# Performance work log

Hardware: AMD Instinct MI355X
Metric: run time of the kernel (lower is better)

The kernel has to match this reference:

```python
import jax, jax.numpy as jnp
import numpy as np

PRUNE = 5      # prune_range from __init__
NEG = -1e30    # finite stand-in for -inf (avoids NaN grads)


def setup_inputs() -> dict:
    B, T, U, V = 8, 200, 200, 512
    key = jax.random.key(0)
    k1, k2, k3, k4 = jax.random.split(key, 4)
    logits = jax.random.normal(k1, (B, T, U, V), dtype=jnp.float32)
    log_probs = jax.nn.log_softmax(logits, axis=-1)  # module expects log_softmax output
    targets = jax.random.randint(k2, (B, U), 1, V, dtype=jnp.int32)  # 0 is blank
    # t_len <= T-1 required since DP indexes log_probs[b, t_len, ...]
    logit_lengths = jax.random.randint(k3, (B,), 120, T, dtype=jnp.int32)
    # diagonal band pruning => need |u_len - t_len| <= PRUNE for finite loss
    target_lengths = logit_lengths - jax.random.randint(k4, (B,), 0, PRUNE + 1, dtype=jnp.int32)
    return {
        "log_probs": log_probs,
        "targets": targets,
        "logit_lengths": logit_lengths,
        "target_lengths": target_lengths,
    }


def _alpha_grid(lp, tgt):
    """Banded RNNT forward DP for one sample.

    lp: (T, U, V) log-probs, tgt: (U,) int labels.
    Returns alpha grid of shape (T, U); alpha[t, u] matches the torch loop
    (cells outside the band u in [t-P, t+P] are NEG).
    """
    T, U, V = lp.shape
    u = jnp.arange(U)
    # label log-prob at (t, u): lp[t, u, tgt[u]]
    L = jnp.take_along_axis(lp, jnp.broadcast_to(tgt[None, :, None], (T, U, 1)), axis=2)[..., 0]  # (T, U)
    pb = lp[:, :, 0]  # blank log-probs (T, U)
    # exclusive cumsum of label scores along u: ecum[t, u] = sum_{j<u} L[t, j]
    ecum = jnp.concatenate([jnp.zeros((T, 1), lp.dtype), jnp.cumsum(L[:, :-1], axis=1)], axis=1)

    # row t = 0: alpha[0, u] = sum_{j<u} L[0, j], band u <= PRUNE
    a0 = jnp.where(u <= PRUNE, ecum[0], NEG)

    def step(prev, x):
        t, pbr, ec = x
        band = (u >= t - PRUNE) & (u <= t + PRUNE)
        # blank transition: alpha[t-1, u] + lp[t-1, u, blank]
        A = jnp.where(band, prev + pbr, NEG)
        # label recursion a[u] = logaddexp(A[u], a[u-1] + L[t, u-1]) solved in
        # closed form: a[u] = ec[u] + logcumsumexp_k<=u (A[k] - ec[k])
        a = ec + jax.lax.cumlogsumexp(A - ec, axis=0)
        a = jnp.where(band, a, NEG)
        return a, a

    ts = jnp.arange(1, T)
    _, rows = jax.lax.scan(step, a0, (ts, pb[:-1], ecum[1:]))
    return jnp.concatenate([a0[None], rows], axis=0)  # (T, U)


def reference(log_probs, targets, logit_lengths, target_lengths):
    alphas = jax.vmap(_alpha_grid)(log_probs, targets)  # (B, T, U)
    B = log_probs.shape[0]
    loss = -alphas[jnp.arange(B), logit_lengths, target_lengths]
    return loss.mean()  # reduction='mean'
```

## Files before the change

kernel.cpp:

```cpp
#include <hip/hip_runtime.h>
#include <math.h>

#define TT 200
#define UU 200
#define VV 512
#define BB 8
#define NEGF (-1e30f)
#define PSTRIDE 212
#define ROWS_PER 25

#define WS_P2   0
#define WS_MAXE 27136
#define WS_BASE 28736

#define DPP_QUAD_XOR1       0xB1
#define DPP_QUAD_XOR2       0x4E
#define DPP_ROW_SHL1        0x101
#define DPP_ROW_SHR1        0x111
#define DPP_ROW_SHR2        0x112
#define DPP_ROW_SHR4        0x114
#define DPP_ROW_SHR8        0x118
#define DPP_ROW_MIRROR      0x140
#define DPP_ROW_HALF_MIRROR 0x141

template<int CTRL, bool ZERO>
__device__ __forceinline__ float fdpp(float src) {
    return __int_as_float(__builtin_amdgcn_update_dpp(
        __float_as_int(src), __float_as_int(src), CTRL, 0xF, 0xF, ZERO));
}

__device__ __forceinline__ float max16(float x) {
    x = fmaxf(x, fdpp<DPP_QUAD_XOR1, true>(x));
    x = fmaxf(x, fdpp<DPP_QUAD_XOR2, true>(x));
    x = fmaxf(x, fdpp<DPP_ROW_HALF_MIRROR, true>(x));
    x = fmaxf(x, fdpp<DPP_ROW_MIRROR, true>(x));
    return x;
}

__device__ __forceinline__ float sum16(float x) {
    x += fdpp<DPP_QUAD_XOR1, true>(x);
    x += fdpp<DPP_QUAD_XOR2, true>(x);
    x += fdpp<DPP_ROW_HALF_MIRROR, true>(x);
    x += fdpp<DPP_ROW_MIRROR, true>(x);
    return x;
}

__device__ __forceinline__ float scan16(float x) {
    x += fdpp<DPP_ROW_SHR1, true>(x);
    x += fdpp<DPP_ROW_SHR2, true>(x);
    x += fdpp<DPP_ROW_SHR4, true>(x);
    x += fdpp<DPP_ROW_SHR8, true>(x);
    return x;
}

__global__ __launch_bounds__(256) void rnnt_stage1(
    const float* __restrict__ lp,
    const int* __restrict__ targets,
    const int* __restrict__ logit_lengths,
    const int* __restrict__ target_lengths,
    float* __restrict__ ws)
{
    __shared__ float Ls[26][16];
    __shared__ float Ps[26][16];
    __shared__ float Ce[26 * 16];
    __shared__ int   tgt_s[UU];

    const int blk   = blockIdx.x;
    const int b     = blk >> 3;
    const int slice = blk & 7;
    const int t0    = slice * ROWS_PER;
    const int rlo   = (slice == 0) ? 0 : t0 - 1;
    const int nrows = ROWS_PER + (slice ? 1 : 0);
    const int tid   = threadIdx.x;
    const float LOG2E = 1.4426950408889634f;

    const float* __restrict__ lpb = lp + (size_t)b * TT * UU * VV;

    if (tid < UU) tgt_s[tid] = targets[b * UU + tid];
    __syncthreads();

    #pragma unroll
    for (int it = 0; it < 3; ++it) {
        int idx  = tid + it * 256;
        bool live = idx < nrows * 24;
        int tl = idx / 24;
        int r  = idx - tl * 24;
        bool isL = r < 12;
        int l = isL ? r : r - 12;
        int t = rlo + tl;
        int u = t + l + (isL ? -5 : -4);
        bool ok = live && (u >= 0) && (u < UU);
        float val = 0.0f;
        if (ok) {
            int v = isL ? tgt_s[u] : 0;
            val = lpb[((size_t)t * UU + u) * VV + v] * LOG2E;
        }
        if (live) {
            if (isL) Ls[tl][l] = val;
            else     Ps[tl][l] = val;
        }
    }
    __syncthreads();

    const int g = tid >> 4;
    const int l = tid & 15;

    for (int tl = g; tl < nrows; tl += 16) {
        float lv = (l < 12) ? Ls[tl][l] : 0.0f;
        float cin = scan16(lv);
        Ce[tl * 16 + l] = cin - lv;
    }
    __syncthreads();

    for (int tl = 1 + g; tl < nrows; tl += 16) {
        int t = rlo + tl;
        int u = t - 5 + l;
        bool vcur  = (l <= 10) && (u >= 0) && (u < UU);
        bool vprev = (l + 1 <= 10) && (u >= 0) && (u < UU);
        float cpn = Ce[(tl - 1) * 16 + ((l + 1) & 15)];
        float ps  = (l < 12) ? Ps[tl - 1][l] : 0.0f;
        float cec = Ce[tl * 16 + l];
        float E = vcur ? (cpn + ps - cec) : NEGF;
        float mE = max16(E);
        float p2 = __builtin_amdgcn_exp2f(E - mE);
        if (!vprev) p2 = 0.0f;
        ws[WS_P2 + ((size_t)(b * 16 + l)) * PSTRIDE + (t - 1)] = p2;
        if (l == 0) ws[WS_MAXE + b * 200 + t] = mE;
    }

    const int tlen = logit_lengths[b];
    const int ulen = target_lengths[b];
    if (tid == 0 && tlen >= t0 && tlen < t0 + ROWS_PER) {
        int lstar = ulen - tlen + 5;
        ws[WS_BASE + b] = Ce[(tlen - rlo) * 16 + lstar];
    }
}

__global__ __launch_bounds__(128) void rnnt_stage2(
    const int* __restrict__ logit_lengths,
    const int* __restrict__ target_lengths,
    const float* __restrict__ ws,
    float* __restrict__ out)
{
    __shared__ float red[2];
    const int tid = threadIdx.x;
    const int s = tid >> 4;
    const int l = tid & 15;

    const int tlen = logit_lengths[s];
    const int ulen = target_lengths[s];

    float facc = 0.0f;
    const float* __restrict__ me = ws + WS_MAXE + s * 200;
    for (int t = 1 + l; t <= tlen; t += 16) facc += me[t];
    float F = sum16(facc);

    const float* __restrict__ rowp = ws + WS_P2 + (size_t)(s * 16 + l) * PSTRIDE;

    float Q = (l >= 5 && l <= 10) ? 1.0f : 0.0f;
    int Msum = 0;
    const int nfull = tlen >> 3;

#define STEP(PV) do {                                \
        float sq_ = fdpp<DPP_ROW_SHL1, true>(Q);     \
        Q = scan16(sq_ * (PV));                      \
    } while (0)

    float4 A0 = *(const float4*)(rowp + 0);
    float4 B0 = *(const float4*)(rowp + 4);
    float4 A1 = *(const float4*)(rowp + 8);
    float4 B1 = *(const float4*)(rowp + 12);

    for (int c = 0; c < nfull; ++c) {
        float4 A2 = *(const float4*)(rowp + 8 * c + 16);
        float4 B2 = *(const float4*)(rowp + 8 * c + 20);
        STEP(A0.x); STEP(A0.y); STEP(A0.z); STEP(A0.w);
        STEP(B0.x); STEP(B0.y); STEP(B0.z); STEP(B0.w);
        float mq = max16(Q);
        int ex;
        frexpf(mq, &ex);
        Q = ldexpf(Q, -ex);
        Msum += ex;
        A0 = A1; B0 = B1; A1 = A2; B1 = B2;
    }
    int r = tlen & 7;
    if (r >= 1) STEP(A0.x);
    if (r >= 2) STEP(A0.y);
    if (r >= 3) STEP(A0.z);
    if (r >= 4) STEP(A0.w);
    if (r >= 5) STEP(B0.x);
    if (r >= 6) STEP(B0.y);
    if (r >= 7) STEP(B0.z);
#undef STEP

    int lstar = ulen - tlen + 5;
    float contrib = 0.0f;
    if (l == lstar)
        contrib = ws[WS_BASE + s] + F + (float)Msum + __builtin_amdgcn_logf(Q);
    #pragma unroll
    for (int d = 32; d; d >>= 1) contrib += __shfl_xor(contrib, d, 64);
    if ((tid & 63) == 0) red[tid >> 6] = contrib;
    __syncthreads();
    if (tid == 0) {
        const float LN2 = 0.6931471805599453f;
        out[0] = -(red[0] + red[1]) * (LN2 / (float)BB);
    }
}

extern "C" void kernel_launch(void* const* d_in, const int* in_sizes, int n_in,
                              void* d_out, int out_size, void* d_ws, size_t ws_size,
                              hipStream_t stream) {
    const float* lp  = (const float*)d_in[0];
    const int* tgt   = (const int*)d_in[1];
    const int* llen  = (const int*)d_in[2];
    const int* tlen  = (const int*)d_in[3];
    float* out = (float*)d_out;
    float* wsf = (float*)d_ws;
    (void)in_sizes; (void)n_in; (void)out_size; (void)ws_size;

    rnnt_stage1<<<dim3(BB * 8), 256, 0, stream>>>(lp, tgt, llen, tlen, wsf);
    rnnt_stage2<<<dim3(1), 128, 0, stream>>>(llen, tlen, wsf, out);
}
```

Measured before the change: 26.78 us.

## Precompute 8-step banded transfer matrices in parallel and chain them in stage 2

Stage 1 now runs 25 blocks per sample, each covering 8 time rows. Each block also builds the 16x16 banded product of 8 consecutive per-row transfer steps by propagating unit vectors. Stage 2 is a single serial block; instead of 200 dependent scan steps it applies 24 precomputed matrices with DPP-shifted multiply-adds, prefetching three blocks ahead, then finishes the remainder rows with scans. This shortens the serial dependency chain at the cost of more stage-1 blocks, a larger workspace and heavy register use in stage 2.

Measured after the change: 28.21 us (median of 2 runs). 1.05x slower.

```diff
diff --git a/kernel.cpp b/kernel.cpp
--- a/kernel.cpp
+++ b/kernel.cpp
@@ -7,11 +7,13 @@
 #define BB 8
 #define NEGF (-1e30f)
 #define PSTRIDE 212
-#define ROWS_PER 25
+#define NBLK 24
+#define NC   25
 
 #define WS_P2   0
-#define WS_MAXE 27136
-#define WS_BASE 28736
+#define WS_MAXE (WS_P2 + BB*16*PSTRIDE)
+#define WS_BASE (WS_MAXE + BB*200)
+#define WS_PROD (WS_BASE + BB)
 
 #define DPP_QUAD_XOR1       0xB1
 #define DPP_QUAD_XOR2       0x4E
@@ -53,6 +55,41 @@
     return x;
 }
 
+template<int R>
+__device__ __forceinline__ float shifted(float q) {
+    if constexpr (R == 8) return q;
+    else if constexpr (R > 8) return fdpp<0x110 + (R - 8), true>(q);
+    else return fdpp<0x100 + (8 - R), true>(q);
+}
+
+__device__ __forceinline__ float applyP(const float P[24], float q) {
+    float a0 = P[8] * q;
+    float a1 = P[0] * shifted<0>(q);   float a2 = P[1] * shifted<1>(q);
+    float a3 = P[2] * shifted<2>(q);   a0 += P[3] * shifted<3>(q);
+    a1 += P[4] * shifted<4>(q);        a2 += P[5] * shifted<5>(q);
+    a3 += P[6] * shifted<6>(q);        a0 += P[7] * shifted<7>(q);
+    a1 += P[9] * shifted<9>(q);        a2 += P[10] * shifted<10>(q);
+    a3 += P[11] * shifted<11>(q);      a0 += P[12] * shifted<12>(q);
+    a1 += P[13] * shifted<13>(q);      a2 += P[14] * shifted<14>(q);
+    a3 += P[15] * shifted<15>(q);      a0 += P[16] * shifted<16>(q);
+    a1 += P[17] * shifted<17>(q);      a2 += P[18] * shifted<18>(q);
+    a3 += P[19] * shifted<19>(q);      a0 += P[20] * shifted<20>(q);
+    a1 += P[21] * shifted<21>(q);      a2 += P[22] * shifted<22>(q);
+    a3 += P[23] * shifted<23>(q);
+    return (a0 + a1) + (a2 + a3);
+}
+
+__device__ __forceinline__ void loadblk(float P[24], const float* __restrict__ pbase,
+                                        int c, int l) {
+    #pragma unroll
+    for (int r = 0; r < 24; ++r) {
+        int j = l + 8 - r;
+        int jj = min(max(j, 0), 15);
+        float v = pbase[c * 256 + jj * 16 + l];
+        P[r] = (j >= 0 && j < 16) ? v : 0.0f;
+    }
+}
+
 __global__ __launch_bounds__(256) void rnnt_stage1(
     const float* __restrict__ lp,
     const int* __restrict__ targets,
@@ -60,18 +97,18 @@
     const int* __restrict__ target_lengths,
     float* __restrict__ ws)
 {
-    __shared__ float Ls[26][16];
-    __shared__ float Ps[26][16];
-    __shared__ float Ce[26 * 16];
+    __shared__ float Ls[9][16];
+    __shared__ float Ps[9][16];
+    __shared__ float CeS[9][16];
+    __shared__ __align__(16) float P2T[16][8];
     __shared__ int   tgt_s[UU];
 
-    const int blk   = blockIdx.x;
-    const int b     = blk >> 3;
-    const int slice = blk & 7;
-    const int t0    = slice * ROWS_PER;
-    const int rlo   = (slice == 0) ? 0 : t0 - 1;
-    const int nrows = ROWS_PER + (slice ? 1 : 0);
-    const int tid   = threadIdx.x;
+    const int blk = blockIdx.x;
+    const int b   = blk / NC;
+    const int c   = blk - b * NC;
+    const int r0  = 8 * c;
+    const int nrows = (c == NBLK) ? 8 : 9;
+    const int tid = threadIdx.x;
     const float LOG2E = 1.4426950408889634f;
 
     const float* __restrict__ lpb = lp + (size_t)b * TT * UU * VV;
@@ -79,61 +116,70 @@
     if (tid < UU) tgt_s[tid] = targets[b * UU + tid];
     __syncthreads();
 
-    #pragma unroll
-    for (int it = 0; it < 3; ++it) {
-        int idx  = tid + it * 256;
-        bool live = idx < nrows * 24;
-        int tl = idx / 24;
-        int r  = idx - tl * 24;
+    if (tid < nrows * 24) {
+        int tl = tid / 24;
+        int r  = tid - tl * 24;
         bool isL = r < 12;
-        int l = isL ? r : r - 12;
-        int t = rlo + tl;
-        int u = t + l + (isL ? -5 : -4);
-        bool ok = live && (u >= 0) && (u < UU);
+        int li = isL ? r : r - 12;
+        int t  = r0 + tl;
+        int u  = t + li + (isL ? -5 : -4);
         float val = 0.0f;
-        if (ok) {
+        if (u >= 0 && u < UU) {
             int v = isL ? tgt_s[u] : 0;
             val = lpb[((size_t)t * UU + u) * VV + v] * LOG2E;
         }
-        if (live) {
-            if (isL) Ls[tl][l] = val;
-            else     Ps[tl][l] = val;
-        }
+        if (isL) Ls[tl][li] = val;
+        else     Ps[tl][li] = val;
     }
     __syncthreads();
 
     const int g = tid >> 4;
     const int l = tid & 15;
 
-    for (int tl = g; tl < nrows; tl += 16) {
-        float lv = (l < 12) ? Ls[tl][l] : 0.0f;
+    if (g < nrows) {
+        float lv = (l < 12) ? Ls[g][l] : 0.0f;
         float cin = scan16(lv);
-        Ce[tl * 16 + l] = cin - lv;
-    }
-    __syncthreads();
-
-    for (int tl = 1 + g; tl < nrows; tl += 16) {
-        int t = rlo + tl;
+        CeS[g][l] = cin - lv;
+    }
+    __syncthreads();
+
+    if (g >= 1 && g < nrows) {
+        int t = r0 + g;
         int u = t - 5 + l;
         bool vcur  = (l <= 10) && (u >= 0) && (u < UU);
         bool vprev = (l + 1 <= 10) && (u >= 0) && (u < UU);
-        float cpn = Ce[(tl - 1) * 16 + ((l + 1) & 15)];
-        float ps  = (l < 12) ? Ps[tl - 1][l] : 0.0f;
-        float cec = Ce[tl * 16 + l];
+        float cpn = CeS[g - 1][(l + 1) & 15];
+        float ps  = (l < 12) ? Ps[g - 1][l] : 0.0f;
+        float cec = CeS[g][l];
         float E = vcur ? (cpn + ps - cec) : NEGF;
         float mE = max16(E);
         float p2 = __builtin_amdgcn_exp2f(E - mE);
         if (!vprev) p2 = 0.0f;
-        ws[WS_P2 + ((size_t)(b * 16 + l)) * PSTRIDE + (t - 1)] = p2;
+        ws[WS_P2 + (size_t)(b * 16 + l) * PSTRIDE + (t - 1)] = p2;
         if (l == 0) ws[WS_MAXE + b * 200 + t] = mE;
-    }
-
-    const int tlen = logit_lengths[b];
-    const int ulen = target_lengths[b];
-    if (tid == 0 && tlen >= t0 && tlen < t0 + ROWS_PER) {
-        int lstar = ulen - tlen + 5;
-        ws[WS_BASE + b] = Ce[(tlen - rlo) * 16 + lstar];
-    }
+        if (c < NBLK) P2T[l][g - 1] = p2;
+    }
+
+    const int TL = logit_lengths[b];
+    const int UL = target_lengths[b];
+    if (tid == 0 && ((TL - 1) >> 3) == c)
+        ws[WS_BASE + b] = CeS[TL - r0][UL - TL + 5];
+
+    if (c == NBLK) return;
+    __syncthreads();
+
+    float4 pa  = *(const float4*)&P2T[l][0];
+    float4 pbv = *(const float4*)&P2T[l][4];
+    float x = (l == g) ? 1.0f : 0.0f;
+    x = scan16(fdpp<DPP_ROW_SHL1, true>(x) * pa.x);
+    x = scan16(fdpp<DPP_ROW_SHL1, true>(x) * pa.y);
+    x = scan16(fdpp<DPP_ROW_SHL1, true>(x) * pa.z);
+    x = scan16(fdpp<DPP_ROW_SHL1, true>(x) * pa.w);
+    x = scan16(fdpp<DPP_ROW_SHL1, true>(x) * pbv.x);
+    x = scan16(fdpp<DPP_ROW_SHL1, true>(x) * pbv.y);
+    x = scan16(fdpp<DPP_ROW_SHL1, true>(x) * pbv.z);
+    x = scan16(fdpp<DPP_ROW_SHL1, true>(x) * pbv.w);
+    ws[WS_PROD + ((size_t)(b * NBLK + c) * 16 + g) * 16 + l] = x;
 }
 
 __global__ __launch_bounds__(128) void rnnt_stage2(
@@ -147,56 +193,61 @@
     const int s = tid >> 4;
     const int l = tid & 15;
 
-    const int tlen = logit_lengths[s];
-    const int ulen = target_lengths[s];
+    const int TL = logit_lengths[s];
+    const int UL = target_lengths[s];
+    const int nfull = TL >> 3;
+    const int rt = TL & 7;
+
+    const float* __restrict__ rowp = ws + WS_P2 + (size_t)(s * 16 + l) * PSTRIDE;
+    float4 TA = *(const float4*)(rowp + 8 * nfull);
+    float4 TB = *(const float4*)(rowp + 8 * nfull + 4);
 
     float facc = 0.0f;
     const float* __restrict__ me = ws + WS_MAXE + s * 200;
-    for (int t = 1 + l; t <= tlen; t += 16) facc += me[t];
+    for (int t = 1 + l; t <= TL; t += 16) facc += me[t];
     float F = sum16(facc);
 
-    const float* __restrict__ rowp = ws + WS_P2 + (size_t)(s * 16 + l) * PSTRIDE;
+    const float* __restrict__ pbase = ws + WS_PROD + (size_t)s * NBLK * 256;
+
+    float Pb0[24], Pb1[24], Pb2[24], Pb3[24];
+    loadblk(Pb0, pbase, 0, l);
+    loadblk(Pb1, pbase, 1, l);
+    loadblk(Pb2, pbase, 2, l);
 
     float Q = (l >= 5 && l <= 10) ? 1.0f : 0.0f;
-    int Msum = 0;
-    const int nfull = tlen >> 3;
-
-#define STEP(PV) do {                                \
-        float sq_ = fdpp<DPP_ROW_SHL1, true>(Q);     \
-        Q = scan16(sq_ * (PV));                      \
+    float qs = Q;
+    int Msum = 0, mcap = 0;
+
+#define ITER(C, CUR, NXT) do {                                        \
+        if ((C) + 3 < NBLK) loadblk(NXT, pbase, (C) + 3, l);          \
+        Q = applyP(CUR, Q);                                           \
+        if (((C) & 1) == 1) {                                         \
+            float mq = max16(Q); int ex;                              \
+            frexpf(mq, &ex); Q = ldexpf(Q, -ex); Msum += ex;          \
+        }                                                             \
+        if ((C) == nfull - 1) { qs = Q; mcap = Msum; }                \
     } while (0)
 
-    float4 A0 = *(const float4*)(rowp + 0);
-    float4 B0 = *(const float4*)(rowp + 4);
-    float4 A1 = *(const float4*)(rowp + 8);
-    float4 B1 = *(const float4*)(rowp + 12);
-
-    for (int c = 0; c < nfull; ++c) {
-        float4 A2 = *(const float4*)(rowp + 8 * c + 16);
-        float4 B2 = *(const float4*)(rowp + 8 * c + 20);
-        STEP(A0.x); STEP(A0.y); STEP(A0.z); STEP(A0.w);
-        STEP(B0.x); STEP(B0.y); STEP(B0.z); STEP(B0.w);
-        float mq = max16(Q);
-        int ex;
-        frexpf(mq, &ex);
-        Q = ldexpf(Q, -ex);
-        Msum += ex;
-        A0 = A1; B0 = B1; A1 = A2; B1 = B2;
-    }
-    int r = tlen & 7;
-    if (r >= 1) STEP(A0.x);
-    if (r >= 2) STEP(A0.y);
-    if (r >= 3) STEP(A0.z);
-    if (r >= 4) STEP(A0.w);
-    if (r >= 5) STEP(B0.x);
-    if (r >= 6) STEP(B0.y);
-    if (r >= 7) STEP(B0.z);
-#undef STEP
-
-    int lstar = ulen - tlen + 5;
+    ITER(0,  Pb0, Pb3); ITER(1,  Pb1, Pb0); ITER(2,  Pb2, Pb1); ITER(3,  Pb3, Pb2);
+    ITER(4,  Pb0, Pb3); ITER(5,  Pb1, Pb0); ITER(6,  Pb2, Pb1); ITER(7,  Pb3, Pb2);
+    ITER(8,  Pb0, Pb3); ITER(9,  Pb1, Pb0); ITER(10, Pb2, Pb1); ITER(11, Pb3, Pb2);
+    ITER(12, Pb0, Pb3); ITER(13, Pb1, Pb0); ITER(14, Pb2, Pb1); ITER(15, Pb3, Pb2);
+    ITER(16, Pb0, Pb3); ITER(17, Pb1, Pb0); ITER(18, Pb2, Pb1); ITER(19, Pb3, Pb2);
+    ITER(20, Pb0, Pb3); ITER(21, Pb1, Pb0); ITER(22, Pb2, Pb1); ITER(23, Pb3, Pb2);
+#undef ITER
+
+    if (rt >= 1) qs = scan16(fdpp<DPP_ROW_SHL1, true>(qs) * TA.x);
+    if (rt >= 2) qs = scan16(fdpp<DPP_ROW_SHL1, true>(qs) * TA.y);
+    if (rt >= 3) qs = scan16(fdpp<DPP_ROW_SHL1, true>(qs) * TA.z);
+    if (rt >= 4) qs = scan16(fdpp<DPP_ROW_SHL1, true>(qs) * TA.w);
+    if (rt >= 5) qs = scan16(fdpp<DPP_ROW_SHL1, true>(qs) * TB.x);
+    if (rt >= 6) qs = scan16(fdpp<DPP_ROW_SHL1, true>(qs) * TB.y);
+    if (rt >= 7) qs = scan16(fdpp<DPP_ROW_SHL1, true>(qs) * TB.z);
+
+    int lstar = UL - TL + 5;
     float contrib = 0.0f;
     if (l == lstar)
-        contrib = ws[WS_BASE + s] + F + (float)Msum + __builtin_amdgcn_logf(Q);
+        contrib = ws[WS_BASE + s] + F + (float)mcap + __builtin_amdgcn_logf(qs);
     #pragma unroll
     for (int d = 32; d; d >>= 1) contrib += __shfl_xor(contrib, d, 64);
     if ((tid & 63) == 0) red[tid >> 6] = contrib;
@@ -218,6 +269,6 @@
     float* wsf = (float*)d_ws;
     (void)in_sizes; (void)n_in; (void)out_size; (void)ws_size;
 
-    rnnt_stage1<<<dim3(BB * 8), 256, 0, stream>>>(lp, tgt, llen, tlen, wsf);
+    rnnt_stage1<<<dim3(BB * NC), 256, 0, stream>>>(lp, tgt, llen, tlen, wsf);
     rnnt_stage2<<<dim3(1), 128, 0, stream>>>(llen, tlen, wsf, out);
 }
```
